# Kernel optimization log

Measured on AMD Instinct MI355X. Metric: run time of the kernel, lower is better.

The kernel has to match this reference:

```python
import jax, jax.numpy as jnp
import numpy as np

NH = 16  # num_heads


def _ln(x, eps=1e-6):
    m = x.mean(-1, keepdims=True)
    v = ((x - m) ** 2).mean(-1, keepdims=True)
    return (x - m) * jax.lax.rsqrt(v + eps)


def _mod(z, sh, sc):
    return z * (1 + sc[:, None, :]) + sh[:, None, :]


def _attn(q, k, v, out_w, out_b, nh=NH):
    B, S, E = q.shape
    hd = E // nh
    q = q.reshape(B, S, nh, hd)
    k = k.reshape(B, -1, nh, hd)
    v = v.reshape(B, -1, nh, hd)
    s = jnp.einsum('bqhd,bkhd->bhqk', q, k) / float(np.sqrt(hd))
    a = jax.nn.softmax(s, axis=-1)
    o = jnp.einsum('bhqk,bkhd->bqhd', a, v).reshape(B, S, E)
    return o @ out_w.T + out_b


def setup_inputs() -> dict:
    key = jax.random.key(0)
    ks = jax.random.split(key, 40)
    E, L, Ne, I, p, C, clip, Kd = 1024, 2, 8, 4096, 2, 4, 768, 1536
    N = (64 // p) ** 2
    n = lambda k, shape, s=0.02: (jax.random.normal(k, shape, jnp.float32) * s)
    inp = {
        'x': jax.random.normal(ks[0], (2, C, 64, 64), jnp.float32),
        't': jax.random.uniform(ks[1], (2,), jnp.float32) * 1000.0,
        'clip_vec': jax.random.normal(ks[2], (2, clip), jnp.float32),
        'qwen_context': jax.random.normal(ks[3], (2, 256, Kd), jnp.float32),
        'conv_w': n(ks[4], (E, C, p, p)),
        'conv_b': n(ks[5], (E,)),
        'pos_embed': n(ks[6], (1, N, E)),
        'tmlp_w1': n(ks[7], (256, 256)), 'tmlp_b1': n(ks[8], (256,)),
        'tmlp_w2': n(ks[9], (256, 256)), 'tmlp_b2': n(ks[10], (256,)),
        'cond_w': n(ks[11], (E, 256 + clip)), 'cond_b': n(ks[12], (E,)),
        'ada_w': n(ks[13], (L, 9 * E, E)), 'ada_b': n(ks[14], (L, 9 * E)),
        'sa_in_w': n(ks[15], (L, 3 * E, E)), 'sa_in_b': n(ks[16], (L, 3 * E)),
        'sa_out_w': n(ks[17], (L, E, E)), 'sa_out_b': n(ks[18], (L, E)),
        'ca_q_w': n(ks[19], (L, E, E)), 'ca_k_w': n(ks[20], (L, E, Kd)),
        'ca_v_w': n(ks[21], (L, E, Kd)), 'ca_in_b': n(ks[22], (L, 3 * E)),
        'ca_out_w': n(ks[23], (L, E, E)), 'ca_out_b': n(ks[24], (L, E)),
        'gate_w': n(ks[25], (L, Ne, E)), 'gate_b': n(ks[26], (L, Ne)),
        'e_w1': n(ks[27], (L, Ne, I, E)), 'e_b1': n(ks[28], (L, Ne, I)),
        'e_w2': n(ks[29], (L, Ne, E, I)), 'e_b2': n(ks[30], (L, Ne, E)),
        'fin_w': n(ks[31], (p * p * C, E)), 'fin_b': n(ks[32], (p * p * C,)),
    }
    return inp


def reference(x, t, clip_vec, qwen_context, conv_w, conv_b, pos_embed,
              tmlp_w1, tmlp_b1, tmlp_w2, tmlp_b2, cond_w, cond_b,
              ada_w, ada_b, sa_in_w, sa_in_b, sa_out_w, sa_out_b,
              ca_q_w, ca_k_w, ca_v_w, ca_in_b, ca_out_w, ca_out_b,
              gate_w, gate_b, e_w1, e_b1, e_w2, e_b2, fin_w, fin_b):
    B, C, H, W = x.shape
    E, p = conv_w.shape[0], conv_w.shape[-1]
    h, w = H // p, W // p
    # patch-embed conv (kernel==stride) as unfold + matmul
    patches = x.reshape(B, C, h, p, w, p).transpose(0, 2, 4, 1, 3, 5).reshape(B, h * w, C * p * p)
    xt = patches @ conv_w.reshape(E, -1).T + conv_b + pos_embed
    # sinusoidal timestep embedding (dim 256)
    half = 128
    freqs = jnp.exp(jnp.arange(half, dtype=jnp.float32) * (-np.log(10000.0) / (half - 1)))
    te = t[:, None] * freqs[None, :]
    te = jnp.concatenate([jnp.sin(te), jnp.cos(te)], -1)
    te = jax.nn.silu(te @ tmlp_w1.T + tmlp_b1) @ tmlp_w2.T + tmlp_b2
    c = jnp.concatenate([te, clip_vec], -1) @ cond_w.T + cond_b  # [B,E]
    depth = ada_w.shape[0]
    for i in range(depth):
        pr = jax.nn.silu(c) @ ada_w[i].T + ada_b[i]
        sh_sa, sc_sa, g_sa, sh_ca, sc_ca, g_ca, sh_m, sc_m, g_m = jnp.split(pr, 9, axis=1)
        # self-attention
        xn = _mod(_ln(xt), sh_sa, sc_sa)
        qkv = xn @ sa_in_w[i].T + sa_in_b[i]
        q, k, v = jnp.split(qkv, 3, axis=-1)
        xt = xt + g_sa[:, None, :] * _attn(q, k, v, sa_out_w[i], sa_out_b[i])
        # cross-attention with separate q/k/v projections
        xn = _mod(_ln(xt), sh_ca, sc_ca)
        q = xn @ ca_q_w[i].T + ca_in_b[i, :E]
        k = qwen_context @ ca_k_w[i].T + ca_in_b[i, E:2 * E]
        v = qwen_context @ ca_v_w[i].T + ca_in_b[i, 2 * E:]
        xt = xt + g_ca[:, None, :] * _attn(q, k, v, ca_out_w[i], ca_out_b[i])
        # top-2 sparse MoE (dense-combine formulation: zero weight for unrouted experts)
        xn = _mod(_ln(xt), sh_m, sc_m)
        probs = jax.nn.softmax(xn @ gate_w[i].T + gate_b[i], axis=-1)
        tw, ti = jax.lax.top_k(probs, 2)
        tw = tw / (tw.sum(-1, keepdims=True) + 1e-6)
        wd = (jax.nn.one_hot(ti, probs.shape[-1], dtype=xn.dtype) * tw[..., None]).sum(-2)  # [B,S,Ne]
        hid = jax.nn.gelu(jnp.einsum('bsd,eid->bsei', xn, e_w1[i]) + e_b1[i], approximate=True)
        y = jnp.einsum('bsei,eoi->bseo', hid, e_w2[i]) + e_b2[i]
        moe = jnp.einsum('bseo,bse->bso', y, wd)
        xt = xt + g_m[:, None, :] * moe
    # final layer + unpatchify (nhwpqc->nchpwq)
    xt = _ln(xt) @ fin_w.T + fin_b
    out = xt.reshape(B, h, w, p, p, C).transpose(0, 5, 1, 3, 2, 4).reshape(B, C, h * p, w * p)
    return out
```

## Files before the change

### kernel.cpp

```cpp
#include <hip/hip_runtime.h>
#include <hip/hip_bf16.h>

#define B_ 2
#define S_ 1024
#define E_ 1024
#define NHEAD 16
#define NE 8
#define II 4096
#define KD 1536
#define CLIP_ 768
#define TOK (B_*S_)

typedef short bf16x8 __attribute__((ext_vector_type(8)));
typedef float f32x4 __attribute__((ext_vector_type(4)));

__device__ __forceinline__ float siluf(float x){ return x/(1.f+expf(-x)); }
__device__ __forceinline__ float geluf(float x){
    float x3 = x*x*x;
    return 0.5f*x*(1.f+tanhf(0.7978845608028654f*(x+0.044715f*x3)));
}
__device__ __forceinline__ unsigned short h16(float x){
    union { __hip_bfloat16 b; unsigned short u; } c;
    c.b = __float2bfloat16(x);
    return c.u;
}
__device__ __forceinline__ unsigned pk2(float a, float b){
    return (unsigned)h16(a) | ((unsigned)h16(b)<<16);
}
__device__ __forceinline__ void sp(float a, unsigned& hb, unsigned& lb){
    unsigned short h = h16(a);
    float r = a - __uint_as_float(((unsigned)h)<<16);
    hb = h; lb = h16(r);
}

union U8 { unsigned u[4]; bf16x8 v; uint4 q; };

__global__ void k_patch_embed(const float* __restrict__ x, const float* __restrict__ cw,
                              const float* __restrict__ cb, const float* __restrict__ pos,
                              float* __restrict__ xt){
    int token = blockIdx.x;
    int b = token >> 10, n = token & 1023;
    int hh = n >> 5, ww = n & 31;
    __shared__ float patch[16];
    int tid = threadIdx.x;
    if (tid < 16){
        int c = tid >> 2, py = (tid >> 1) & 1, px = tid & 1;
        patch[tid] = x[(((size_t)b*4 + c)*64 + hh*2+py)*64 + ww*2+px];
    }
    __syncthreads();
    for (int e = tid; e < E_; e += 256){
        float acc = cb[e];
        #pragma unroll
        for (int j=0;j<16;j++) acc += patch[j]*cw[e*16+j];
        xt[(size_t)token*E_ + e] = acc + pos[(size_t)n*E_ + e];
    }
}

__global__ void k_time_cond(const float* __restrict__ t, const float* __restrict__ clip,
                            const float* __restrict__ w1, const float* __restrict__ b1,
                            const float* __restrict__ w2, const float* __restrict__ b2,
                            const float* __restrict__ cw, const float* __restrict__ cbias,
                            float* __restrict__ silu_c){
    int b = blockIdx.x, tid = threadIdx.x;
    __shared__ float te[256], h1[256], te2[256];
    if (tid < 128){
        float f = expf((float)tid * (-9.210340371976184f/127.f));
        float a = t[b]*f;
        te[tid]     = sinf(a);
        te[tid+128] = cosf(a);
    }
    __syncthreads();
    {
        float acc = b1[tid];
        const float* wr = w1 + (size_t)tid*256;
        for (int k=0;k<256;k++) acc += te[k]*wr[k];
        h1[tid] = siluf(acc);
    }
    __syncthreads();
    {
        float acc = b2[tid];
        const float* wr = w2 + (size_t)tid*256;
        for (int k=0;k<256;k++) acc += h1[k]*wr[k];
        te2[tid] = acc;
    }
    __syncthreads();
    const float* cl = clip + (size_t)b*CLIP_;
    for (int e = tid; e < E_; e += 256){
        float acc = cbias[e];
        const float* wr = cw + (size_t)e*1024;
        for (int k=0;k<256;k++)  acc += te2[k]*wr[k];
        for (int k=0;k<CLIP_;k++) acc += cl[k]*wr[256+k];
        silu_c[b*E_+e] = siluf(acc);
    }
}

__global__ void k_ada2(const float* __restrict__ sic, const float* __restrict__ aw,
                       const float* __restrict__ ab, float* __restrict__ pr){
    int row = blockIdx.x*4 + (threadIdx.x>>6);
    int lane = threadIdx.x & 63;
    const float* w = aw + (size_t)row*1024;
    float a0 = 0.f, a1 = 0.f;
    #pragma unroll
    for (int it=0; it<4; it++){
        int k = it*256 + lane*4;
        float4 wv = *(const float4*)(w+k);
        float4 x0 = *(const float4*)(sic+k);
        float4 x1 = *(const float4*)(sic+1024+k);
        a0 += wv.x*x0.x + wv.y*x0.y + wv.z*x0.z + wv.w*x0.w;
        a1 += wv.x*x1.x + wv.y*x1.y + wv.z*x1.z + wv.w*x1.w;
    }
    #pragma unroll
    for (int off=32; off; off>>=1){ a0 += __shfl_down(a0,off); a1 += __shfl_down(a1,off); }
    if (lane==0){
        float bb = ab[row];
        pr[row] = a0 + bb;
        pr[9*E_ + row] = a1 + bb;
    }
}

__global__ void k_ln_mod(const float* __restrict__ src, float* __restrict__ dst32,
                         unsigned short* __restrict__ dsth, unsigned short* __restrict__ dstl,
                         const float* __restrict__ pr, int shc, int scc){
    int token = blockIdx.x, tid = threadIdx.x;
    int b = token >> 10;
    const float* row = src + (size_t)token*E_;
    float4 v = *(const float4*)(row + tid*4);
    float s = v.x+v.y+v.z+v.w;
    float ss = v.x*v.x+v.y*v.y+v.z*v.z+v.w*v.w;
    #pragma unroll
    for (int off=32; off; off>>=1){ s += __shfl_down(s,off); ss += __shfl_down(ss,off); }
    __shared__ float rs_[4], rss_[4];
    int wid = tid >> 6;
    if ((tid&63)==0){ rs_[wid]=s; rss_[wid]=ss; }
    __syncthreads();
    s  = rs_[0]+rs_[1]+rs_[2]+rs_[3];
    ss = rss_[0]+rss_[1]+rss_[2]+rss_[3];
    float mean = s*(1.f/1024.f);
    float rstd = rsqrtf(ss*(1.f/1024.f) - mean*mean + 1e-6f);
    const float* shv = pr + b*9*E_ + shc*E_;
    const float* scv = pr + b*9*E_ + scc*E_;
    int e = tid*4;
    float o[4];
    float4 sc4 = *(const float4*)(scv+e);
    float4 sh4 = *(const float4*)(shv+e);
    o[0] = (v.x-mean)*rstd*(1.f+sc4.x) + sh4.x;
    o[1] = (v.y-mean)*rstd*(1.f+sc4.y) + sh4.y;
    o[2] = (v.z-mean)*rstd*(1.f+sc4.z) + sh4.z;
    o[3] = (v.w-mean)*rstd*(1.f+sc4.w) + sh4.w;
    if (dst32) *(float4*)(dst32 + (size_t)token*E_ + e) = make_float4(o[0],o[1],o[2],o[3]);
    unsigned hu[2], lu[2];
    {
        unsigned h0,l0,h1,l1;
        sp(o[0],h0,l0); sp(o[1],h1,l1);
        hu[0]=h0|(h1<<16); lu[0]=l0|(l1<<16);
        sp(o[2],h0,l0); sp(o[3],h1,l1);
        hu[1]=h0|(h1<<16); lu[1]=l0|(l1<<16);
    }
    *(uint2*)(dsth + (size_t)token*E_ + e) = make_uint2(hu[0],hu[1]);
    *(uint2*)(dstl + (size_t)token*E_ + e) = make_uint2(lu[0],lu[1]);
}

__global__ void k_split4(const float* __restrict__ src, unsigned short* __restrict__ hp,
                         unsigned short* __restrict__ lp, int n4){
    int i = blockIdx.x*256 + threadIdx.x;
    if (i >= n4) return;
    float4 v = *(const float4*)(src + i*4);
    unsigned h0,l0,h1,l1,h2,l2,h3,l3;
    sp(v.x,h0,l0); sp(v.y,h1,l1); sp(v.z,h2,l2); sp(v.w,h3,l3);
    *(uint2*)(hp + i*4) = make_uint2(h0|(h1<<16), h2|(h3<<16));
    *(uint2*)(lp + i*4) = make_uint2(l0|(l1<<16), l2|(l3<<16));
}

template<int MOE, int EPI, int GATHER, int TERMS>
__global__ __launch_bounds__(256) void k_mm(
    const unsigned short* __restrict__ Ahpp, const unsigned short* __restrict__ Alpp, int lda,
    const float* __restrict__ Wp, int ldw,
    const float* __restrict__ biasp, int bstride,
    void* __restrict__ Cp, void* __restrict__ Cp2, int ldc,
    int M, int N, int K,
    const float* __restrict__ pr, int gch,
    const int* __restrict__ cnt, const int* __restrict__ offs,
    const int* __restrict__ list)
{
    constexpr int NPL = (TERMS==3) ? 2 : 1;
    int e  = MOE ? blockIdx.z : 0;
    int Mm = MOE ? cnt[e] : M;
    int bm = blockIdx.y*128;
    if (MOE && bm >= Mm) return;
    int o0 = MOE ? offs[e] : 0;
    int bn = blockIdx.x*128;
    const float* W = Wp + (size_t)e*N*ldw;
    const float* bias = biasp + (size_t)e*bstride;

    __shared__ __align__(16) unsigned short As_[2][NPL][128*40];
    __shared__ __align__(16) unsigned short Bs_[2][NPL][128*40];

    int tid = threadIdx.x;
    int lane = tid & 63, wid = tid >> 6;
    int wm = wid >> 1, wn = wid & 1;

    int srow = tid >> 1, shalf = tid & 1;
    int sbase = srow*40 + shalf*16;
    int amr = bm + srow; if (amr >= Mm) amr = Mm - 1;
    int arow;
    if (MOE) arow = GATHER ? list[o0 + amr] : (o0 + amr);
    else     arow = amr;
    const unsigned short* Ahp = Ahpp + (size_t)arow*lda + shalf*16;
    const unsigned short* Alp = (TERMS==3) ? (Alpp + (size_t)arow*lda + shalf*16) : nullptr;
    const float* Bf = W + (size_t)(bn + srow)*ldw + shalf*16;

    float fB[16];
    uint4 aH0, aH1, aL0, aL1;

    auto LOAD = [&](int k0){
        aH0 = *(const uint4*)(Ahp+k0);
        aH1 = *(const uint4*)(Ahp+k0+8);
        if (TERMS==3){
            aL0 = *(const uint4*)(Alp+k0);
            aL1 = *(const uint4*)(Alp+k0+8);
        }
        *(float4*)(fB+0)  = *(const float4*)(Bf+k0+0);
        *(float4*)(fB+4)  = *(const float4*)(Bf+k0+4);
        *(float4*)(fB+8)  = *(const float4*)(Bf+k0+8);
        *(float4*)(fB+12) = *(const float4*)(Bf+k0+12);
    };
    auto STAGE = [&](int buf){
        *(uint4*)&As_[buf][0][sbase]   = aH0;
        *(uint4*)&As_[buf][0][sbase+8] = aH1;
        if (TERMS==3){
            *(uint4*)&As_[buf][NPL-1][sbase]   = aL0;
            *(uint4*)&As_[buf][NPL-1][sbase+8] = aL1;
        }
        if (TERMS==3){
            unsigned hb2[8], lb2[8];
            #pragma unroll
            for (int i=0;i<8;i++){
                unsigned h0,l0,h1,l1;
                sp(fB[2*i],h0,l0); sp(fB[2*i+1],h1,l1);
                hb2[i]=h0|(h1<<16); lb2[i]=l0|(l1<<16);
            }
            *(uint4*)&Bs_[buf][0][sbase]   = make_uint4(hb2[0],hb2[1],hb2[2],hb2[3]);
            *(uint4*)&Bs_[buf][0][sbase+8] = make_uint4(hb2[4],hb2[5],hb2[6],hb2[7]);
            *(uint4*)&Bs_[buf][NPL-1][sbase]   = make_uint4(lb2[0],lb2[1],lb2[2],lb2[3]);
            *(uint4*)&Bs_[buf][NPL-1][sbase+8] = make_uint4(lb2[4],lb2[5],lb2[6],lb2[7]);
        } else {
            unsigned hb2[8];
            #pragma unroll
            for (int i=0;i<8;i++) hb2[i] = pk2(fB[2*i],fB[2*i+1]);
            *(uint4*)&Bs_[buf][0][sbase]   = make_uint4(hb2[0],hb2[1],hb2[2],hb2[3]);
            *(uint4*)&Bs_[buf][0][sbase+8] = make_uint4(hb2[4],hb2[5],hb2[6],hb2[7]);
        }
    };

    f32x4 acc[4][4];
    #pragma unroll
    for (int m=0;m<4;m++)
        #pragma unroll
        for (int n=0;n<4;n++) acc[m][n] = (f32x4){0.f,0.f,0.f,0.f};

    int fr = lane & 15, fko = (lane>>4)*8, fr4 = (lane>>4)*4;

    LOAD(0);
    STAGE(0);
    __syncthreads();
    int cur = 0;
    for (int k0=0; k0<K; k0+=32){
        bool nxt = (k0+32) < K;
        if (nxt) LOAD(k0+32);
        bf16x8 ah[4], bh[4], al[4], bl[4];
        #pragma unroll
        for (int m=0;m<4;m++){
            int off = (wm*64 + m*16 + fr)*40 + fko;
            ah[m] = *(const bf16x8*)&As_[cur][0][off];
            if (TERMS==3) al[m] = *(const bf16x8*)&As_[cur][NPL-1][off];
        }
        #pragma unroll
        for (int n=0;n<4;n++){
            int off = (wn*64 + n*16 + fr)*40 + fko;
            bh[n] = *(const bf16x8*)&Bs_[cur][0][off];
            if (TERMS==3) bl[n] = *(const bf16x8*)&Bs_[cur][NPL-1][off];
        }
        #pragma unroll
        for (int m=0;m<4;m++)
            #pragma unroll
            for (int n=0;n<4;n++){
                acc[m][n] = __builtin_amdgcn_mfma_f32_16x16x32_bf16(ah[m], bh[n], acc[m][n], 0, 0, 0);
                if (TERMS==3){
                    acc[m][n] = __builtin_amdgcn_mfma_f32_16x16x32_bf16(ah[m], bl[n], acc[m][n], 0, 0, 0);
                    acc[m][n] = __builtin_amdgcn_mfma_f32_16x16x32_bf16(al[m], bh[n], acc[m][n], 0, 0, 0);
                }
            }
        if (nxt) STAGE(cur^1);
        __syncthreads();
        cur ^= 1;
    }

    #pragma unroll
    for (int m=0;m<4;m++){
        #pragma unroll
        for (int j=0;j<4;j++){
            int row = bm + wm*64 + m*16 + fr4 + j;
            if (row >= Mm) continue;
            #pragma unroll
            for (int n=0;n<4;n++){
                int col = bn + wn*64 + n*16 + fr;
                float v = acc[m][n][j] + bias[col];
                if (EPI==0){
                    ((float*)Cp)[(size_t)row*ldc + col] = v;
                } else if (EPI==1){
                    int bb = row >> 10;
                    ((float*)Cp)[(size_t)row*ldc + col] += pr[bb*9*E_ + gch*E_ + col] * v;
                } else if (EPI==2){
                    if (TERMS==3){
                        unsigned hb, lb; sp(geluf(v), hb, lb);
                        ((unsigned short*)Cp )[(size_t)(o0+row)*ldc + col] = (unsigned short)hb;
                        ((unsigned short*)Cp2)[(size_t)(o0+row)*ldc + col] = (unsigned short)lb;
                    } else {
                        ((unsigned short*)Cp )[(size_t)(o0+row)*ldc + col] = h16(geluf(v));
                    }
                } else {
                    ((float*)Cp)[(size_t)(o0+row)*ldc + col] = v;
                }
            }
        }
    }
}

__global__ __launch_bounds__(256) void k_attn_m(
    const float* __restrict__ qp, int qstride,
    const float* __restrict__ kp, const float* __restrict__ vp, int kvstride,
    unsigned short* __restrict__ oph, unsigned short* __restrict__ opl,
    int ostride, int Sq, int Sk, float scale)
{
    __shared__ __align__(16) unsigned short Kh[64*72];
    __shared__ __align__(16) unsigned short Kl[64*72];
    __shared__ __align__(16) unsigned V_i[64*70];
    __shared__ __align__(16) unsigned short P_[4][2][16*72];

    int tid = threadIdx.x, lane = tid & 63, wid = tid >> 6;
    int g = lane >> 4, fr = lane & 15;
    int h = blockIdx.y, b = blockIdx.z;
    int qbase = blockIdx.x*64;

    bf16x8 qh[2], ql[2];
    {
        const float* qr = qp + (size_t)(b*Sq + qbase + wid*16 + fr)*qstride + h*64;
        #pragma unroll
        for (int ds=0; ds<2; ds++){
            float f[8];
            *(float4*)(f+0) = *(const float4*)(qr + ds*32 + g*8);
            *(float4*)(f+4) = *(const float4*)(qr + ds*32 + g*8 + 4);
            U8 uh, ul;
            #pragma unroll
            for (int i=0;i<4;i++){
                unsigned h0,l0,h1,l1;
                sp(f[2*i]*scale, h0,l0); sp(f[2*i+1]*scale, h1,l1);
                uh.u[i] = h0|(h1<<16); ul.u[i] = l0|(l1<<16);
            }
            qh[ds] = uh.v; ql[ds] = ul.v;
        }
    }

    float m_run = -1e30f, l_run = 0.f;
    f32x4 oacc[4];
    #pragma unroll
    for (int dt=0;dt<4;dt++) oacc[dt] = (f32x4){0.f,0.f,0.f,0.f};

    unsigned short* PhW = &P_[wid][0][0];
    unsigned short* PlW = &P_[wid][1][0];

    for (int kt0 = 0; kt0 < Sk; kt0 += 64){
        __syncthreads();
        {
            int srow = tid >> 2, d0 = (tid & 3) << 4;
            size_t grow = (size_t)(b*Sk + kt0 + srow)*kvstride + h*64 + d0;
            {
                const float* srcp = kp + grow;
                float f[16];
                *(float4*)(f+0)  = *(const float4*)(srcp+0);
                *(float4*)(f+4)  = *(const float4*)(srcp+4);
                *(float4*)(f+8)  = *(const float4*)(srcp+8);
                *(float4*)(f+12) = *(const float4*)(srcp+12);
                U8 uh0, uh1, ul0, ul1;
                #pragma unroll
                for (int i=0;i<4;i++){
                    unsigned a0,b0,a1,b1;
                    sp(f[2*i],a0,b0); sp(f[2*i+1],a1,b1);
                    uh0.u[i] = a0|(a1<<16); ul0.u[i] = b0|(b1<<16);
                }
                #pragma unroll
                for (int i=0;i<4;i++){
                    unsigned a0,b0,a1,b1;
                    sp(f[8+2*i],a0,b0); sp(f[8+2*i+1],a1,b1);
                    uh1.u[i] = a0|(a1<<16); ul1.u[i] = b0|(b1<<16);
                }
                int base = srow*72 + d0;
                *(uint4*)&Kh[base]     = uh0.q;
                *(uint4*)&Kh[base + 8] = uh1.q;
                *(uint4*)&Kl[base]     = ul0.q;
                *(uint4*)&Kl[base + 8] = ul1.q;
            }
            {
                const float* srcp = vp + grow;
                float f[16];
                *(float4*)(f+0)  = *(const float4*)(srcp+0);
                *(float4*)(f+4)  = *(const float4*)(srcp+4);
                *(float4*)(f+8)  = *(const float4*)(srcp+8);
                *(float4*)(f+12) = *(const float4*)(srcp+12);
                int base = srow*70 + d0;
                #pragma unroll
                for (int i4=0;i4<4;i4++){
                    U8 u;
                    #pragma unroll
                    for (int i=0;i<4;i++){
                        unsigned hb, lb; sp(f[4*i4+i], hb, lb);
                        u.u[i] = hb | (lb<<16);
                    }
                    *(uint2*)&V_i[base + i4*4]     = make_uint2(u.u[0], u.u[1]);
                    *(uint2*)&V_i[base + i4*4 + 2] = make_uint2(u.u[2], u.u[3]);
                }
            }
        }
        __syncthreads();

        f32x4 st[4];
        #pragma unroll
        for (int kt=0;kt<4;kt++) st[kt] = (f32x4){0.f,0.f,0.f,0.f};
        #pragma unroll
        for (int ds=0; ds<2; ds++){
            #pragma unroll
            for (int kt=0;kt<4;kt++){
                int row = kt*16 + fr;
                int so = row*72 + ds*32 + g*8;
                bf16x8 kh  = *(const bf16x8*)&Kh[so];
                bf16x8 klo = *(const bf16x8*)&Kl[so];
                st[kt] = __builtin_amdgcn_mfma_f32_16x16x32_bf16(kh, qh[ds], st[kt], 0,0,0);
                st[kt] = __builtin_amdgcn_mfma_f32_16x16x32_bf16(kh, ql[ds], st[kt], 0,0,0);
                st[kt] = __builtin_amdgcn_mfma_f32_16x16x32_bf16(klo, qh[ds], st[kt], 0,0,0);
            }
        }

        float pmax = -1e30f;
        #pragma unroll
        for (int kt=0;kt<4;kt++)
            #pragma unroll
            for (int r=0;r<4;r++) pmax = fmaxf(pmax, st[kt][r]);
        pmax = fmaxf(pmax, __shfl_xor(pmax, 16));
        pmax = fmaxf(pmax, __shfl_xor(pmax, 32));
        float mnew = fmaxf(m_run, pmax);
        float p[4][4]; float psum = 0.f;
        #pragma unroll
        for (int kt=0;kt<4;kt++)
            #pragma unroll
            for (int r=0;r<4;r++){ float pv = expf(st[kt][r] - mnew); p[kt][r] = pv; psum += pv; }
        psum += __shfl_xor(psum, 16);
        psum += __shfl_xor(psum, 32);
        float corr = expf(m_run - mnew);
        l_run = l_run*corr + psum;
        m_run = mnew;
        #pragma unroll
        for (int j=0;j<4;j++){
            float cj = __shfl(corr, g*4 + j);
            #pragma unroll
            for (int dt=0;dt<4;dt++) oacc[dt][j] *= cj;
        }

        #pragma unroll
        for (int kt=0;kt<4;kt++){
            unsigned h0,l0,h1,l1,h2,l2,h3,l3;
            sp(p[kt][0],h0,l0); sp(p[kt][1],h1,l1);
            sp(p[kt][2],h2,l2); sp(p[kt][3],h3,l3);
            int base = fr*72 + kt*16 + g*4;
            *(unsigned*)&PhW[base]     = h0|(h1<<16);
            *(unsigned*)&PhW[base + 2] = h2|(h3<<16);
            *(unsigned*)&PlW[base]     = l0|(l1<<16);
            *(unsigned*)&PlW[base + 2] = l2|(l3<<16);
        }

        #pragma unroll
        for (int ks=0; ks<2; ks++){
            int pso = fr*72 + ks*32 + g*8;
            bf16x8 ph = *(const bf16x8*)&PhW[pso];
            bf16x8 pl = *(const bf16x8*)&PlW[pso];
            #pragma unroll
            for (int dt=0; dt<4; dt++){
                unsigned w[8];
                #pragma unroll
                for (int j=0;j<8;j++){
                    int row = ks*32 + g*8 + j;
                    w[j] = V_i[row*70 + dt*16 + fr];
                }
                U8 vh, vl;
                #pragma unroll
                for (int i=0;i<4;i++){
                    vh.u[i] = (w[2*i] & 0xffffu) | (w[2*i+1] << 16);
                    vl.u[i] = (w[2*i] >> 16)     | (w[2*i+1] & 0xffff0000u);
                }
                oacc[dt] = __builtin_amdgcn_mfma_f32_16x16x32_bf16(ph, vh.v, oacc[dt], 0,0,0);
                oacc[dt] = __builtin_amdgcn_mfma_f32_16x16x32_bf16(ph, vl.v, oacc[dt], 0,0,0);
                oacc[dt] = __builtin_amdgcn_mfma_f32_16x16x32_bf16(pl, vh.v, oacc[dt], 0,0,0);
            }
        }
    }

    float linv = 1.f / l_run;
    #pragma unroll
    for (int j=0;j<4;j++){
        float lj = __shfl(linv, g*4 + j);
        int row = qbase + wid*16 + g*4 + j;
        size_t obase = (size_t)(b*Sq + row)*ostride + h*64;
        #pragma unroll
        for (int dt=0;dt<4;dt++){
            unsigned hb, lb; sp(oacc[dt][j]*lj, hb, lb);
            oph[obase + dt*16 + fr] = (unsigned short)hb;
            opl[obase + dt*16 + fr] = (unsigned short)lb;
        }
    }
}

__global__ void k_route(const float* __restrict__ xn, const float* __restrict__ gw,
                        const float* __restrict__ gb, int* __restrict__ i01,
                        float* __restrict__ w01, int* __restrict__ cnt){
    int token = blockIdx.x, lane = threadIdx.x;
    const float* row = xn + (size_t)token*E_;
    float part[8] = {0,0,0,0,0,0,0,0};
    for (int k = lane; k < E_; k += 64){
        float xv = row[k];
        #pragma unroll
        for (int e=0;e<8;e++) part[e] += xv*gw[e*E_+k];
    }
    #pragma unroll
    for (int e=0;e<8;e++){
        #pragma unroll
        for (int off=32; off; off>>=1) part[e] += __shfl_down(part[e], off);
    }
    if (lane==0){
        float lg[8]; float mx = -1e30f;
        #pragma unroll
        for (int e=0;e<8;e++){ lg[e] = part[e]+gb[e]; if (lg[e]>mx) mx = lg[e]; }
        float sum = 0.f;
        #pragma unroll
        for (int e=0;e<8;e++){ lg[e] = expf(lg[e]-mx); sum += lg[e]; }
        int a0 = 0;
        #pragma unroll
        for (int e=1;e<8;e++) if (lg[e] > lg[a0]) a0 = e;
        int a1 = (a0==0)?1:0;
        #pragma unroll
        for (int e=0;e<8;e++) if (e!=a0 && lg[e] > lg[a1]) a1 = e;
        float p0 = lg[a0]/sum, p1 = lg[a1]/sum;
        float inv = 1.f/(p0+p1+1e-6f);
        i01[token*2+0]=a0; i01[token*2+1]=a1;
        w01[token*2+0]=p0*inv; w01[token*2+1]=p1*inv;
        atomicAdd(&cnt[a0],1); atomicAdd(&cnt[a1],1);
    }
}

__global__ void k_scan(const int* __restrict__ cnt, int* __restrict__ offs, int* __restrict__ curs){
    if (threadIdx.x==0 && blockIdx.x==0){
        int o = 0;
        for (int e=0;e<8;e++){ offs[e]=o; curs[e]=o; o += cnt[e]; }
    }
}

__global__ void k_place(const int* __restrict__ i01,
                        int* __restrict__ curs, int* __restrict__ list,
                        int* __restrict__ t2s){
    int t = blockIdx.x*256 + threadIdx.x;
    if (t >= TOK) return;
    #pragma unroll
    for (int s=0;s<2;s++){
        int e = i01[t*2+s];
        int p = atomicAdd(&curs[e],1);
        list[p] = t;
        t2s[t*2+s] = p;
    }
}

__global__ void k_moe_combine2(float* __restrict__ xt, const float* __restrict__ yslot,
                               const int* __restrict__ t2s, const float* __restrict__ w01,
                               const float* __restrict__ pr){
    int idx = blockIdx.x*256 + threadIdx.x;
    int token = idx >> 10, n = idx & 1023;
    int b = token >> 10;
    int s0 = t2s[token*2], s1 = t2s[token*2+1];
    float mo = w01[token*2]*yslot[(size_t)s0*E_+n] + w01[token*2+1]*yslot[(size_t)s1*E_+n];
    xt[idx] += pr[b*9*E_ + 8*E_ + n]*mo;
}

__global__ void k_final(const float* __restrict__ xt, const float* __restrict__ fw,
                        const float* __restrict__ fb, float* __restrict__ out){
    int token = blockIdx.x, tid = threadIdx.x;
    int b = token >> 10, n = token & 1023, hh = n >> 5, ww = n & 31;
    const float* row = xt + (size_t)token*E_;
    float4 v = *(const float4*)(row + tid*4);
    float s = v.x+v.y+v.z+v.w;
    float ss = v.x*v.x+v.y*v.y+v.z*v.z+v.w*v.w;
    #pragma unroll
    for (int off=32; off; off>>=1){ s += __shfl_down(s,off); ss += __shfl_down(ss,off); }
    __shared__ float rs_[4], rss_[4];
    int wid = tid >> 6;
    if ((tid&63)==0){ rs_[wid]=s; rss_[wid]=ss; }
    __syncthreads();
    s  = rs_[0]+rs_[1]+rs_[2]+rs_[3];
    ss = rss_[0]+rss_[1]+rss_[2]+rss_[3];
    float mean = s*(1.f/1024.f);
    float rstd = rsqrtf(ss*(1.f/1024.f) - mean*mean + 1e-6f);
    __shared__ float xl[1024];
    int e = tid*4;
    xl[e+0]=(v.x-mean)*rstd; xl[e+1]=(v.y-mean)*rstd;
    xl[e+2]=(v.z-mean)*rstd; xl[e+3]=(v.w-mean)*rstd;
    __syncthreads();
    int o = tid & 15, seg = tid >> 4;
    float part = 0.f;
    const float* wr = fw + (size_t)o*E_ + seg*64;
    const float* xr = xl + seg*64;
    #pragma unroll 8
    for (int j=0;j<64;j++) part += xr[j]*wr[j];
    __shared__ float ps[16][17];
    ps[seg][o] = part;
    __syncthreads();
    if (tid < 16){
        float acc = fb[tid];
        #pragma unroll
        for (int s2=0;s2<16;s2++) acc += ps[s2][tid];
        int py = tid>>3, px = (tid>>2)&1, ch = tid&3;
        out[(((size_t)b*4+ch)*64 + hh*2+py)*64 + ww*2+px] = acc;
    }
}

extern "C" void kernel_launch(void* const* d_in, const int* in_sizes, int n_in,
                              void* d_out, int out_size, void* d_ws, size_t ws_size,
                              hipStream_t stream){
    const float* x        = (const float*)d_in[0];
    const float* t        = (const float*)d_in[1];
    const float* clip     = (const float*)d_in[2];
    const float* qwen     = (const float*)d_in[3];
    const float* conv_w   = (const float*)d_in[4];
    const float* conv_b   = (const float*)d_in[5];
    const float* pos      = (const float*)d_in[6];
    const float* tw1      = (const float*)d_in[7];
    const float* tb1      = (const float*)d_in[8];
    const float* tw2      = (const float*)d_in[9];
    const float* tb2      = (const float*)d_in[10];
    const float* cond_w   = (const float*)d_in[11];
    const float* cond_b   = (const float*)d_in[12];
    const float* ada_w    = (const float*)d_in[13];
    const float* ada_b    = (const float*)d_in[14];
    const float* sa_in_w  = (const float*)d_in[15];
    const float* sa_in_b  = (const float*)d_in[16];
    const float* sa_out_w = (const float*)d_in[17];
    const float* sa_out_b = (const float*)d_in[18];
    const float* ca_q_w   = (const float*)d_in[19];
    const float* ca_k_w   = (const float*)d_in[20];
    const float* ca_v_w   = (const float*)d_in[21];
    const float* ca_in_b  = (const float*)d_in[22];
    const float* ca_out_w = (const float*)d_in[23];
    const float* ca_out_b = (const float*)d_in[24];
    const float* gate_w   = (const float*)d_in[25];
    const float* gate_b   = (const float*)d_in[26];
    const float* e_w1     = (const float*)d_in[27];
    const float* e_b1     = (const float*)d_in[28];
    const float* e_w2     = (const float*)d_in[29];
    const float* e_b2     = (const float*)d_in[30];
    const float* fin_w    = (const float*)d_in[31];
    const float* fin_b    = (const float*)d_in[32];

    float* ws    = (float*)d_ws;
    float* xt    = ws;
    float* xn    = ws + 2097152;
    float* qkv   = ws + 4194304;
    float* yslot = qkv;
    unsigned short* xnh = (unsigned short*)(ws + 10485760);
    unsigned short* xnl = (unsigned short*)(ws + 11534336);
    unsigned short* obh = (unsigned short*)(ws + 12582912);
    unsigned short* obl = (unsigned short*)(ws + 13631488);
    unsigned short* hidh = (unsigned short*)(ws + 14680064);
    unsigned short* hidl = (unsigned short*)(ws + 23068672);
    unsigned short* qwh = (unsigned short*)(ws + 31457280);
    unsigned short* qwl = (unsigned short*)(ws + 31981568);
    float* kbuf  = ws + 32505856;
    float* vbuf  = ws + 33030144;
    float* pr    = ws + 33554432;
    float* sic   = ws + 33572864;
    float* w01   = ws + 33574912;
    int*   i01   = (int*)(ws + 33579008);
    int*   t2s   = (int*)(ws + 33583104);
    int*   list  = (int*)(ws + 33587200);
    int*   cnt   = (int*)(ws + 33591296);
    int*   offs  = cnt + 8;
    int*   curs  = cnt + 16;

    k_patch_embed<<<TOK,256,0,stream>>>(x, conv_w, conv_b, pos, xt);
    k_time_cond<<<B_,256,0,stream>>>(t, clip, tw1, tb1, tw2, tb2, cond_w, cond_b, sic);
    k_split4<<<(B_*256*KD/4+255)/256,256,0,stream>>>(qwen, qwh, qwl, B_*256*KD/4);

    for (int i=0;i<2;i++){
        k_ada2<<<2304,256,0,stream>>>(sic, ada_w + (size_t)i*9*E_*E_,
                                      ada_b + (size_t)i*9*E_, pr);
        k_ln_mod<<<TOK,256,0,stream>>>(xt, nullptr, xnh, xnl, pr, 0, 1);
        k_mm<0,0,0,3><<<dim3(24,16),256,0,stream>>>(
            xnh, xnl, E_, sa_in_w + (size_t)i*3*E_*E_, E_, sa_in_b + (size_t)i*3*E_, 0,
            qkv, nullptr, 3*E_, TOK, 3*E_, E_, nullptr, 0, nullptr, nullptr, nullptr);
        k_attn_m<<<dim3(16,NHEAD,B_),256,0,stream>>>(qkv, 3*E_, qkv+E_, qkv+2*E_, 3*E_,
                                                     obh, obl, E_, S_, S_, 0.125f);
        k_mm<0,1,0,3><<<dim3(8,16),256,0,stream>>>(
            obh, obl, E_, sa_out_w + (size_t)i*E_*E_, E_, sa_out_b + (size_t)i*E_, 0,
            xt, nullptr, E_, TOK, E_, E_, pr, 2, nullptr, nullptr, nullptr);
        k_ln_mod<<<TOK,256,0,stream>>>(xt, nullptr, xnh, xnl, pr, 3, 4);
        k_mm<0,0,0,3><<<dim3(8,16),256,0,stream>>>(
            xnh, xnl, E_, ca_q_w + (size_t)i*E_*E_, E_, ca_in_b + (size_t)i*3*E_, 0,
            qkv, nullptr, E_, TOK, E_, E_, nullptr, 0, nullptr, nullptr, nullptr);
        k_mm<0,0,0,3><<<dim3(8,4),256,0,stream>>>(
            qwh, qwl, KD, ca_k_w + (size_t)i*E_*KD, KD, ca_in_b + (size_t)i*3*E_ + E_, 0,
            kbuf, nullptr, E_, B_*256, E_, KD, nullptr, 0, nullptr, nullptr, nullptr);
        k_mm<0,0,0,3><<<dim3(8,4),256,0,stream>>>(
            qwh, qwl, KD, ca_v_w + (size_t)i*E_*KD, KD, ca_in_b + (size_t)i*3*E_ + 2*E_, 0,
            vbuf, nullptr, E_, B_*256, E_, KD, nullptr, 0, nullptr, nullptr, nullptr);
        k_attn_m<<<dim3(16,NHEAD,B_),256,0,stream>>>(qkv, E_, kbuf, vbuf, E_,
                                                     obh, obl, E_, S_, 256, 0.125f);
        k_mm<0,1,0,3><<<dim3(8,16),256,0,stream>>>(
            obh, obl, E_, ca_out_w + (size_t)i*E_*E_, E_, ca_out_b + (size_t)i*E_, 0,
            xt, nullptr, E_, TOK, E_, E_, pr, 5, nullptr, nullptr, nullptr);
        k_ln_mod<<<TOK,256,0,stream>>>(xt, xn, xnh, xnl, pr, 6, 7);
        hipMemsetAsync(cnt, 0, 8*sizeof(int), stream);
        k_route<<<TOK,64,0,stream>>>(xn, gate_w + (size_t)i*NE*E_, gate_b + (size_t)i*NE,
                                     i01, w01, cnt);
        k_scan<<<1,64,0,stream>>>(cnt, offs, curs);
        k_place<<<TOK/256,256,0,stream>>>(i01, curs, list, t2s);
        if (i==0){
            k_mm<1,2,1,3><<<dim3(32,32,NE),256,0,stream>>>(
                xnh, xnl, E_, e_w1 + (size_t)i*NE*II*E_, E_, e_b1 + (size_t)i*NE*II, II,
                hidh, hidl, II, 0, II, E_, nullptr, 0, cnt, offs, list);
            k_mm<1,3,0,3><<<dim3(8,32,NE),256,0,stream>>>(
                hidh, hidl, II, e_w2 + (size_t)i*NE*E_*II, II, e_b2 + (size_t)i*NE*E_, E_,
                yslot, nullptr, E_, 0, E_, II, nullptr, 0, cnt, offs, list);
        } else {
            k_mm<1,2,1,1><<<dim3(32,32,NE),256,0,stream>>>(
                xnh, nullptr, E_, e_w1 + (size_t)i*NE*II*E_, E_, e_b1 + (size_t)i*NE*II, II,
                hidh, nullptr, II, 0, II, E_, nullptr, 0, cnt, offs, list);
            k_mm<1,3,0,1><<<dim3(8,32,NE),256,0,stream>>>(
                hidh, nullptr, II, e_w2 + (size_t)i*NE*E_*II, II, e_b2 + (size_t)i*NE*E_, E_,
                yslot, nullptr, E_, 0, E_, II, nullptr, 0, cnt, offs, list);
        }
        k_moe_combine2<<<TOK*E_/256,256,0,stream>>>(xt, yslot, t2s, w01, pr);
    }
    k_final<<<TOK,256,0,stream>>>(xt, fin_w, fin_b, (float*)d_out);
}
```

Measured before the change: 2.154 ms.

## Pre-split K/V into head-major bf16 layouts, split-K expert down-proj, parallelize cond

The QKV and cross-attention K/V projection epilogues now write K and V directly as head-major hi/lo bf16 pairs. The attention kernel can then copy tiles straight into shared memory instead of converting fp32 per tile for every query block. The MoE down-projection uses a 4-way split-K with atomicAdd into a zeroed yslot buffer, giving more blocks to fill the GPU. The conditioning MLP is split into a small time-MLP kernel and a wave-parallel cond kernel. These changes add a memset and atomic traffic and change the fp32 summation order.

```diff
diff --git a/kernel.cpp b/kernel.cpp
--- a/kernel.cpp
+++ b/kernel.cpp
@@ -56,13 +56,12 @@
     }
 }
 
-__global__ void k_time_cond(const float* __restrict__ t, const float* __restrict__ clip,
-                            const float* __restrict__ w1, const float* __restrict__ b1,
-                            const float* __restrict__ w2, const float* __restrict__ b2,
-                            const float* __restrict__ cw, const float* __restrict__ cbias,
-                            float* __restrict__ silu_c){
+__global__ void k_time_mlp(const float* __restrict__ t,
+                           const float* __restrict__ w1, const float* __restrict__ b1,
+                           const float* __restrict__ w2, const float* __restrict__ b2,
+                           float* __restrict__ te2g){
     int b = blockIdx.x, tid = threadIdx.x;
-    __shared__ float te[256], h1[256], te2[256];
+    __shared__ float te[256], h1[256];
     if (tid < 128){
         float f = expf((float)tid * (-9.210340371976184f/127.f));
         float a = t[b]*f;
@@ -81,17 +80,25 @@
         float acc = b2[tid];
         const float* wr = w2 + (size_t)tid*256;
         for (int k=0;k<256;k++) acc += h1[k]*wr[k];
-        te2[tid] = acc;
-    }
-    __syncthreads();
-    const float* cl = clip + (size_t)b*CLIP_;
-    for (int e = tid; e < E_; e += 256){
-        float acc = cbias[e];
-        const float* wr = cw + (size_t)e*1024;
-        for (int k=0;k<256;k++)  acc += te2[k]*wr[k];
-        for (int k=0;k<CLIP_;k++) acc += cl[k]*wr[256+k];
-        silu_c[b*E_+e] = siluf(acc);
-    }
+        te2g[b*256+tid] = acc;
+    }
+}
+
+__global__ void k_cond(const float* __restrict__ te2g, const float* __restrict__ clip,
+                       const float* __restrict__ cw, const float* __restrict__ cb,
+                       float* __restrict__ silu_c){
+    int idx = blockIdx.x*4 + (threadIdx.x>>6);
+    int lane = threadIdx.x & 63;
+    int b = idx >> 10, e = idx & 1023;
+    const float* wr = cw + (size_t)e*1024;
+    float acc = 0.f;
+    for (int k=lane; k<1024; k+=64){
+        float xv = (k<256)? te2g[b*256+k] : clip[b*CLIP_ + k-256];
+        acc += xv*wr[k];
+    }
+    #pragma unroll
+    for (int off=32; off; off>>=1) acc += __shfl_down(acc,off);
+    if (lane==0) silu_c[b*E_+e] = siluf(acc + cb[e]);
 }
 
 __global__ void k_ada2(const float* __restrict__ sic, const float* __restrict__ aw,
@@ -171,13 +178,13 @@
     *(uint2*)(lp + i*4) = make_uint2(l0|(l1<<16), l2|(l3<<16));
 }
 
-template<int MOE, int EPI, int GATHER, int TERMS>
+template<int MOE, int EPI, int GATHER, int TERMS, int SPLITK=1>
 __global__ __launch_bounds__(256) void k_mm(
     const unsigned short* __restrict__ Ahpp, const unsigned short* __restrict__ Alpp, int lda,
     const float* __restrict__ Wp, int ldw,
     const float* __restrict__ biasp, int bstride,
-    void* __restrict__ Cp, void* __restrict__ Cp2, int ldc,
-    int M, int N, int K,
+    void* __restrict__ Cp, void* __restrict__ Cp2, void* __restrict__ Cp3, void* __restrict__ Cp4,
+    int ldc, int M, int N, int K,
     const float* __restrict__ pr, int gch,
     const int* __restrict__ cnt, const int* __restrict__ offs,
     const int* __restrict__ list)
@@ -188,8 +195,11 @@
     int bm = blockIdx.y*128;
     if (MOE && bm >= Mm) return;
     int o0 = MOE ? offs[e] : 0;
-    int bn = blockIdx.x*128;
-    const float* W = Wp + (size_t)e*N*ldw;
+    int nt = gridDim.x / SPLITK;
+    int ntile = blockIdx.x % nt;
+    int kc0 = blockIdx.x / nt;
+    int bn = ntile*128;
+    int kbeg = kc0*(K/SPLITK), kend = kbeg + K/SPLITK;
     const float* bias = biasp + (size_t)e*bstride;
 
     __shared__ __align__(16) unsigned short As_[2][NPL][128*40];
@@ -207,7 +217,7 @@
     else     arow = amr;
     const unsigned short* Ahp = Ahpp + (size_t)arow*lda + shalf*16;
     const unsigned short* Alp = (TERMS==3) ? (Alpp + (size_t)arow*lda + shalf*16) : nullptr;
-    const float* Bf = W + (size_t)(bn + srow)*ldw + shalf*16;
+    const float* Bf = Wp + (size_t)e*N*ldw + (size_t)(bn + srow)*ldw + shalf*16;
 
     float fB[16];
     uint4 aH0, aH1, aL0, aL1;
@@ -260,12 +270,12 @@
 
     int fr = lane & 15, fko = (lane>>4)*8, fr4 = (lane>>4)*4;
 
-    LOAD(0);
+    LOAD(kbeg);
     STAGE(0);
     __syncthreads();
     int cur = 0;
-    for (int k0=0; k0<K; k0+=32){
-        bool nxt = (k0+32) < K;
+    for (int k0=kbeg; k0<kend; k0+=32){
+        bool nxt = (k0+32) < kend;
         if (nxt) LOAD(k0+32);
         bf16x8 ah[4], bh[4], al[4], bl[4];
         #pragma unroll
@@ -304,22 +314,55 @@
             #pragma unroll
             for (int n=0;n<4;n++){
                 int col = bn + wn*64 + n*16 + fr;
-                float v = acc[m][n][j] + bias[col];
+                float bv = (SPLITK==1 || kc0==0) ? bias[col] : 0.f;
+                float v = acc[m][n][j] + bv;
                 if (EPI==0){
                     ((float*)Cp)[(size_t)row*ldc + col] = v;
                 } else if (EPI==1){
                     int bb = row >> 10;
                     ((float*)Cp)[(size_t)row*ldc + col] += pr[bb*9*E_ + gch*E_ + col] * v;
                 } else if (EPI==2){
+                    size_t pi = (size_t)(o0+row)*ldc + col;
                     if (TERMS==3){
                         unsigned hb, lb; sp(geluf(v), hb, lb);
-                        ((unsigned short*)Cp )[(size_t)(o0+row)*ldc + col] = (unsigned short)hb;
-                        ((unsigned short*)Cp2)[(size_t)(o0+row)*ldc + col] = (unsigned short)lb;
+                        ((unsigned short*)Cp )[pi] = (unsigned short)hb;
+                        ((unsigned short*)Cp2)[pi] = (unsigned short)lb;
                     } else {
-                        ((unsigned short*)Cp )[(size_t)(o0+row)*ldc + col] = h16(geluf(v));
+                        ((unsigned short*)Cp )[pi] = h16(geluf(v));
                     }
+                } else if (EPI==3){
+                    if (SPLITK==1)
+                        ((float*)Cp)[(size_t)(o0+row)*ldc + col] = v;
+                    else
+                        atomicAdd(&((float*)Cp)[(size_t)(o0+row)*ldc + col], v);
+                } else if (EPI==4){
+                    if (col < 1024){
+                        ((float*)Cp)[(size_t)row*1024 + col] = v;
+                    } else {
+                        int c2 = col - 1024;
+                        int isv = c2 >> 10;
+                        int cc = c2 & 1023;
+                        int hh2 = cc >> 6, d = cc & 63;
+                        size_t idx = (((size_t)(row>>10)*NHEAD + hh2)*1024 + (row & 1023))*64 + d;
+                        unsigned hb, lb; sp(v, hb, lb);
+                        if (!isv){
+                            ((unsigned short*)Cp2)[idx] = (unsigned short)hb;
+                            ((unsigned short*)Cp3)[idx] = (unsigned short)lb;
+                        } else {
+                            ((unsigned*)Cp4)[idx] = hb | (lb<<16);
+                        }
+                    }
+                } else if (EPI==5){
+                    int hh2 = col >> 6, d = col & 63;
+                    size_t idx = (((size_t)(row>>8)*NHEAD + hh2)*256 + (row & 255))*64 + d;
+                    unsigned hb, lb; sp(v, hb, lb);
+                    ((unsigned short*)Cp )[idx] = (unsigned short)hb;
+                    ((unsigned short*)Cp2)[idx] = (unsigned short)lb;
                 } else {
-                    ((float*)Cp)[(size_t)(o0+row)*ldc + col] = v;
+                    int hh2 = col >> 6, d = col & 63;
+                    size_t idx = (((size_t)(row>>8)*NHEAD + hh2)*256 + (row & 255))*64 + d;
+                    unsigned hb, lb; sp(v, hb, lb);
+                    ((unsigned*)Cp)[idx] = hb | (lb<<16);
                 }
             }
         }
@@ -328,9 +371,10 @@
 
 __global__ __launch_bounds__(256) void k_attn_m(
     const float* __restrict__ qp, int qstride,
-    const float* __restrict__ kp, const float* __restrict__ vp, int kvstride,
+    const unsigned short* __restrict__ Khp, const unsigned short* __restrict__ Klp,
+    const unsigned* __restrict__ Vip,
     unsigned short* __restrict__ oph, unsigned short* __restrict__ opl,
-    int ostride, int Sq, int Sk, float scale)
+    int Sq, int Sk, float scale)
 {
     __shared__ __align__(16) unsigned short Kh[64*72];
     __shared__ __align__(16) unsigned short Kl[64*72];
@@ -341,6 +385,7 @@
     int g = lane >> 4, fr = lane & 15;
     int h = blockIdx.y, b = blockIdx.z;
     int qbase = blockIdx.x*64;
+    size_t bhbase = (size_t)(b*NHEAD + h)*Sk*64;
 
     bf16x8 qh[2], ql[2];
     {
@@ -373,52 +418,19 @@
         __syncthreads();
         {
             int srow = tid >> 2, d0 = (tid & 3) << 4;
-            size_t grow = (size_t)(b*Sk + kt0 + srow)*kvstride + h*64 + d0;
-            {
-                const float* srcp = kp + grow;
-                float f[16];
-                *(float4*)(f+0)  = *(const float4*)(srcp+0);
-                *(float4*)(f+4)  = *(const float4*)(srcp+4);
-                *(float4*)(f+8)  = *(const float4*)(srcp+8);
-                *(float4*)(f+12) = *(const float4*)(srcp+12);
-                U8 uh0, uh1, ul0, ul1;
-                #pragma unroll
-                for (int i=0;i<4;i++){
-                    unsigned a0,b0,a1,b1;
-                    sp(f[2*i],a0,b0); sp(f[2*i+1],a1,b1);
-                    uh0.u[i] = a0|(a1<<16); ul0.u[i] = b0|(b1<<16);
-                }
-                #pragma unroll
-                for (int i=0;i<4;i++){
-                    unsigned a0,b0,a1,b1;
-                    sp(f[8+2*i],a0,b0); sp(f[8+2*i+1],a1,b1);
-                    uh1.u[i] = a0|(a1<<16); ul1.u[i] = b0|(b1<<16);
-                }
-                int base = srow*72 + d0;
-                *(uint4*)&Kh[base]     = uh0.q;
-                *(uint4*)&Kh[base + 8] = uh1.q;
-                *(uint4*)&Kl[base]     = ul0.q;
-                *(uint4*)&Kl[base + 8] = ul1.q;
-            }
-            {
-                const float* srcp = vp + grow;
-                float f[16];
-                *(float4*)(f+0)  = *(const float4*)(srcp+0);
-                *(float4*)(f+4)  = *(const float4*)(srcp+4);
-                *(float4*)(f+8)  = *(const float4*)(srcp+8);
-                *(float4*)(f+12) = *(const float4*)(srcp+12);
-                int base = srow*70 + d0;
-                #pragma unroll
-                for (int i4=0;i4<4;i4++){
-                    U8 u;
-                    #pragma unroll
-                    for (int i=0;i<4;i++){
-                        unsigned hb, lb; sp(f[4*i4+i], hb, lb);
-                        u.u[i] = hb | (lb<<16);
-                    }
-                    *(uint2*)&V_i[base + i4*4]     = make_uint2(u.u[0], u.u[1]);
-                    *(uint2*)&V_i[base + i4*4 + 2] = make_uint2(u.u[2], u.u[3]);
-                }
+            size_t gidx = bhbase + (size_t)(kt0 + srow)*64 + d0;
+            int base = srow*72 + d0;
+            *(uint4*)&Kh[base]   = *(const uint4*)(Khp + gidx);
+            *(uint4*)&Kh[base+8] = *(const uint4*)(Khp + gidx + 8);
+            *(uint4*)&Kl[base]   = *(const uint4*)(Klp + gidx);
+            *(uint4*)&Kl[base+8] = *(const uint4*)(Klp + gidx + 8);
+            const unsigned* vsrc = Vip + gidx;
+            int vb = srow*70 + d0;
+            #pragma unroll
+            for (int i4=0;i4<4;i4++){
+                uint4 u = *(const uint4*)(vsrc + i4*4);
+                *(uint2*)&V_i[vb + i4*4]     = make_uint2(u.x,u.y);
+                *(uint2*)&V_i[vb + i4*4 + 2] = make_uint2(u.z,u.w);
             }
         }
         __syncthreads();
@@ -508,7 +520,7 @@
     for (int j=0;j<4;j++){
         float lj = __shfl(linv, g*4 + j);
         int row = qbase + wid*16 + g*4 + j;
-        size_t obase = (size_t)(b*Sq + row)*ostride + h*64;
+        size_t obase = (size_t)(b*Sq + row)*E_ + h*64;
         #pragma unroll
         for (int dt=0;dt<4;dt++){
             unsigned hb, lb; sp(oacc[dt][j]*lj, hb, lb);
@@ -668,18 +680,19 @@
     float* ws    = (float*)d_ws;
     float* xt    = ws;
     float* xn    = ws + 2097152;
-    float* qkv   = ws + 4194304;
-    float* yslot = qkv;
-    unsigned short* xnh = (unsigned short*)(ws + 10485760);
-    unsigned short* xnl = (unsigned short*)(ws + 11534336);
-    unsigned short* obh = (unsigned short*)(ws + 12582912);
-    unsigned short* obl = (unsigned short*)(ws + 13631488);
+    float* qbuf  = ws + 4194304;
+    unsigned short* Khp = (unsigned short*)(ws + 6291456);
+    unsigned short* Klp = (unsigned short*)(ws + 7340032);
+    unsigned*       Vip = (unsigned*)(ws + 8388608);
+    float* yslot = ws + 4194304;
+    unsigned short* xnh  = (unsigned short*)(ws + 10485760);
+    unsigned short* xnl  = (unsigned short*)(ws + 11534336);
+    unsigned short* obh  = (unsigned short*)(ws + 12582912);
+    unsigned short* obl  = (unsigned short*)(ws + 13631488);
     unsigned short* hidh = (unsigned short*)(ws + 14680064);
     unsigned short* hidl = (unsigned short*)(ws + 23068672);
-    unsigned short* qwh = (unsigned short*)(ws + 31457280);
-    unsigned short* qwl = (unsigned short*)(ws + 31981568);
-    float* kbuf  = ws + 32505856;
-    float* vbuf  = ws + 33030144;
+    unsigned short* qwh  = (unsigned short*)(ws + 31457280);
+    unsigned short* qwl  = (unsigned short*)(ws + 31981568);
     float* pr    = ws + 33554432;
     float* sic   = ws + 33572864;
     float* w01   = ws + 33574912;
@@ -689,58 +702,61 @@
     int*   cnt   = (int*)(ws + 33591296);
     int*   offs  = cnt + 8;
     int*   curs  = cnt + 16;
+    float* te2g  = ws + 33591808;
 
     k_patch_embed<<<TOK,256,0,stream>>>(x, conv_w, conv_b, pos, xt);
-    k_time_cond<<<B_,256,0,stream>>>(t, clip, tw1, tb1, tw2, tb2, cond_w, cond_b, sic);
+    k_time_mlp<<<B_,256,0,stream>>>(t, tw1, tb1, tw2, tb2, te2g);
+    k_cond<<<512,256,0,stream>>>(te2g, clip, cond_w, cond_b, sic);
     k_split4<<<(B_*256*KD/4+255)/256,256,0,stream>>>(qwen, qwh, qwl, B_*256*KD/4);
 
     for (int i=0;i<2;i++){
         k_ada2<<<2304,256,0,stream>>>(sic, ada_w + (size_t)i*9*E_*E_,
                                       ada_b + (size_t)i*9*E_, pr);
         k_ln_mod<<<TOK,256,0,stream>>>(xt, nullptr, xnh, xnl, pr, 0, 1);
-        k_mm<0,0,0,3><<<dim3(24,16),256,0,stream>>>(
+        k_mm<0,4,0,3><<<dim3(24,16),256,0,stream>>>(
             xnh, xnl, E_, sa_in_w + (size_t)i*3*E_*E_, E_, sa_in_b + (size_t)i*3*E_, 0,
-            qkv, nullptr, 3*E_, TOK, 3*E_, E_, nullptr, 0, nullptr, nullptr, nullptr);
-        k_attn_m<<<dim3(16,NHEAD,B_),256,0,stream>>>(qkv, 3*E_, qkv+E_, qkv+2*E_, 3*E_,
-                                                     obh, obl, E_, S_, S_, 0.125f);
+            qbuf, Khp, Klp, Vip, 0, TOK, 3*E_, E_, nullptr, 0, nullptr, nullptr, nullptr);
+        k_attn_m<<<dim3(16,NHEAD,B_),256,0,stream>>>(qbuf, 1024, Khp, Klp, Vip,
+                                                     obh, obl, S_, S_, 0.125f);
         k_mm<0,1,0,3><<<dim3(8,16),256,0,stream>>>(
             obh, obl, E_, sa_out_w + (size_t)i*E_*E_, E_, sa_out_b + (size_t)i*E_, 0,
-            xt, nullptr, E_, TOK, E_, E_, pr, 2, nullptr, nullptr, nullptr);
+            xt, nullptr, nullptr, nullptr, E_, TOK, E_, E_, pr, 2, nullptr, nullptr, nullptr);
         k_ln_mod<<<TOK,256,0,stream>>>(xt, nullptr, xnh, xnl, pr, 3, 4);
         k_mm<0,0,0,3><<<dim3(8,16),256,0,stream>>>(
             xnh, xnl, E_, ca_q_w + (size_t)i*E_*E_, E_, ca_in_b + (size_t)i*3*E_, 0,
-            qkv, nullptr, E_, TOK, E_, E_, nullptr, 0, nullptr, nullptr, nullptr);
-        k_mm<0,0,0,3><<<dim3(8,4),256,0,stream>>>(
+            qbuf, nullptr, nullptr, nullptr, E_, TOK, E_, E_, nullptr, 0, nullptr, nullptr, nullptr);
+        k_mm<0,5,0,3><<<dim3(8,4),256,0,stream>>>(
             qwh, qwl, KD, ca_k_w + (size_t)i*E_*KD, KD, ca_in_b + (size_t)i*3*E_ + E_, 0,
-            kbuf, nullptr, E_, B_*256, E_, KD, nullptr, 0, nullptr, nullptr, nullptr);
-        k_mm<0,0,0,3><<<dim3(8,4),256,0,stream>>>(
+            Khp, Klp, nullptr, nullptr, 0, B_*256, E_, KD, nullptr, 0, nullptr, nullptr, nullptr);
+        k_mm<0,6,0,3><<<dim3(8,4),256,0,stream>>>(
             qwh, qwl, KD, ca_v_w + (size_t)i*E_*KD, KD, ca_in_b + (size_t)i*3*E_ + 2*E_, 0,
-            vbuf, nullptr, E_, B_*256, E_, KD, nullptr, 0, nullptr, nullptr, nullptr);
-        k_attn_m<<<dim3(16,NHEAD,B_),256,0,stream>>>(qkv, E_, kbuf, vbuf, E_,
-                                                     obh, obl, E_, S_, 256, 0.125f);
+            Vip, nullptr, nullptr, nullptr, 0, B_*256, E_, KD, nullptr, 0, nullptr, nullptr, nullptr);
+        k_attn_m<<<dim3(16,NHEAD,B_),256,0,stream>>>(qbuf, E_, Khp, Klp, Vip,
+                                                     obh, obl, S_, 256, 0.125f);
         k_mm<0,1,0,3><<<dim3(8,16),256,0,stream>>>(
             obh, obl, E_, ca_out_w + (size_t)i*E_*E_, E_, ca_out_b + (size_t)i*E_, 0,
-            xt, nullptr, E_, TOK, E_, E_, pr, 5, nullptr, nullptr, nullptr);
+            xt, nullptr, nullptr, nullptr, E_, TOK, E_, E_, pr, 5, nullptr, nullptr, nullptr);
         k_ln_mod<<<TOK,256,0,stream>>>(xt, xn, xnh, xnl, pr, 6, 7);
         hipMemsetAsync(cnt, 0, 8*sizeof(int), stream);
         k_route<<<TOK,64,0,stream>>>(xn, gate_w + (size_t)i*NE*E_, gate_b + (size_t)i*NE,
                                      i01, w01, cnt);
         k_scan<<<1,64,0,stream>>>(cnt, offs, curs);
         k_place<<<TOK/256,256,0,stream>>>(i01, curs, list, t2s);
+        hipMemsetAsync(yslot, 0, (size_t)2*TOK*E_*sizeof(float), stream);
         if (i==0){
             k_mm<1,2,1,3><<<dim3(32,32,NE),256,0,stream>>>(
                 xnh, xnl, E_, e_w1 + (size_t)i*NE*II*E_, E_, e_b1 + (size_t)i*NE*II, II,
-                hidh, hidl, II, 0, II, E_, nullptr, 0, cnt, offs, list);
-            k_mm<1,3,0,3><<<dim3(8,32,NE),256,0,stream>>>(
+                hidh, hidl, nullptr, nullptr, II, 0, II, E_, nullptr, 0, cnt, offs, list);
+            k_mm<1,3,0,3,4><<<dim3(32,32,NE),256,0,stream>>>(
                 hidh, hidl, II, e_w2 + (size_t)i*NE*E_*II, II, e_b2 + (size_t)i*NE*E_, E_,
-                yslot, nullptr, E_, 0, E_, II, nullptr, 0, cnt, offs, list);
+                yslot, nullptr, nullptr, nullptr, E_, 0, E_, II, nullptr, 0, cnt, offs, nullptr);
         } else {
             k_mm<1,2,1,1><<<dim3(32,32,NE),256,0,stream>>>(
                 xnh, nullptr, E_, e_w1 + (size_t)i*NE*II*E_, E_, e_b1 + (size_t)i*NE*II, II,
-                hidh, nullptr, II, 0, II, E_, nullptr, 0, cnt, offs, list);
-            k_mm<1,3,0,1><<<dim3(8,32,NE),256,0,stream>>>(
+                hidh, nullptr, nullptr, nullptr, II, 0, II, E_, nullptr, 0, cnt, offs, list);
+            k_mm<1,3,0,1,4><<<dim3(32,32,NE),256,0,stream>>>(
                 hidh, nullptr, II, e_w2 + (size_t)i*NE*E_*II, II, e_b2 + (size_t)i*NE*E_, E_,
-                yslot, nullptr, E_, 0, E_, II, nullptr, 0, cnt, offs, list);
+                yslot, nullptr, nullptr, nullptr, E_, 0, E_, II, nullptr, 0, cnt, offs, nullptr);
         }
         k_moe_combine2<<<TOK*E_/256,256,0,stream>>>(xt, yslot, t2s, w01, pr);
     }
```

Result: faster. 1.955 ms, median of 2 (-9.2%).
